# Performance work log

Hardware: AMD Instinct MI355X
Metric: run time of the kernel (lower is better)

## Reference

```python
import jax, jax.numpy as jnp
import numpy as np

EPS = 1e-3  # Keras BatchNormalization default epsilon


def _bn(x, gamma, beta, mean, var):
    # inference-mode batchnorm over channel axis 1 of [N,C,T,V]
    s = (gamma * jax.lax.rsqrt(var + EPS)).reshape(1, -1, 1, 1)
    b = (beta - gamma * mean * jax.lax.rsqrt(var + EPS)).reshape(1, -1, 1, 1)
    return x * s + b


def setup_inputs() -> dict:
    key = jax.random.key(0)
    ks = jax.random.split(key, 10)
    N, C, T, V, K, F, KT = 64, 64, 300, 25, 3, 64, 9
    x = jax.random.normal(ks[0], (N, C, T, V), jnp.float32)
    W1 = jax.random.normal(ks[1], (C, F * K), jnp.float32) * 0.05
    b1 = jnp.zeros((F * K,), jnp.float32)
    A = jax.random.normal(ks[2], (K, T, V, V), jnp.float32) * 0.2
    gamma1 = jnp.ones((F,), jnp.float32)
    beta1 = jnp.zeros((F,), jnp.float32)
    mean1 = jax.random.normal(ks[3], (F,), jnp.float32) * 0.1
    var1 = jax.random.uniform(ks[4], (F,), jnp.float32) + 0.5
    Wt = jax.random.normal(ks[5], (KT, 1, F, F), jnp.float32) * 0.05  # HWIO
    bt = jnp.zeros((F,), jnp.float32)
    gamma2 = jnp.ones((F,), jnp.float32)
    beta2 = jnp.zeros((F,), jnp.float32)
    mean2 = jax.random.normal(ks[6], (F,), jnp.float32) * 0.1
    var2 = jax.random.uniform(ks[7], (F,), jnp.float32) + 0.5
    return dict(x=x, W1=W1, b1=b1, A=A, gamma1=gamma1, beta1=beta1,
                mean1=mean1, var1=var1, Wt=Wt, bt=bt, gamma2=gamma2,
                beta2=beta2, mean2=mean2, var2=var2)


def reference(x, W1, b1, A, gamma1, beta1, mean1, var1, Wt, bt,
              gamma2, beta2, mean2, var2):
    N, C, T, V = x.shape
    K = A.shape[0]
    F = W1.shape[1] // K
    # SGTACN: 1x1 conv (channels_first) == channel matmul
    y = jnp.einsum('nctv,cf->nftv', x, W1) + b1.reshape(1, -1, 1, 1)
    y = y.reshape(N, K, F, T, V)
    # spatial graph contraction with learned per-timestep adjacency
    y = jnp.einsum('nkftv,ktvw->nftw', y, A)
    # tgcn: BN -> relu -> temporal conv [9,1] SAME -> BN
    y = jax.nn.relu(_bn(y, gamma1, beta1, mean1, var1))
    y = jax.lax.conv_general_dilated(
        y, Wt, window_strides=(1, 1), padding='SAME',
        dimension_numbers=('NCHW', 'HWIO', 'NCHW')) + bt.reshape(1, -1, 1, 1)
    y = _bn(y, gamma2, beta2, mean2, var2)
    # identity residual (stride=1, no downsample, C_in == filters) + relu
    return jax.nn.relu(y + x)
```

## Files before the change

### kernel.cpp

```cpp
#include <hip/hip_runtime.h>
#include <hip/hip_bf16.h>
#include <stdint.h>

#define EPS 1e-3f

typedef __attribute__((ext_vector_type(8))) short bf16x8;
typedef __attribute__((ext_vector_type(4))) float f32x4;

__device__ inline uint32_t pk2(float a, float b) {
    __hip_bfloat162 p;
    p.x = __float2bfloat16(a);
    p.y = __float2bfloat16(b);
    return *(uint32_t*)&p;
}

__global__ __launch_bounds__(256) void k0_prep_small(
    const float* __restrict__ W1, const float* __restrict__ Wt,
    const float* __restrict__ A,
    uint16_t* __restrict__ W1t, uint16_t* __restrict__ Abf,
    float* __restrict__ csA_g)
{
    int i = blockIdx.x * 256 + threadIdx.x;
    if (i < 12288) {
        int f = i / 192, Kp = i % 192, k = Kp >> 6, c = Kp & 63;
        __hip_bfloat16 b = __float2bfloat16(W1[c * 192 + k * 64 + f]);
        W1t[i] = *(uint16_t*)&b;
    } else if (i < 49152) {
        int j = i - 12288;
        int jj = j & 7, fo = (j >> 3) & 63, kb = j >> 9;
        int kk = kb * 8 + jj, dt = kk >> 6, fi = kk & 63;
        __hip_bfloat16 b = __float2bfloat16(Wt[(dt * 64 + fi) * 64 + fo]);
        Abf[j] = *(uint16_t*)&b;
    } else if (i < 71652) {
        int j = i - 49152;
        int k = j / 7500, r = j % 7500;
        int t = r / 25, w = r % 25;
        float s = 0.f;
        for (int v = 0; v < 25; ++v)
            s += A[((k * 300 + t) * 25 + v) * 25 + w];
        csA_g[j] = s;
    }
}

__global__ __launch_bounds__(256) void k0_prep_At(
    const float* __restrict__ A, uint16_t* __restrict__ At_g)
{
    int i = blockIdx.x * 256 + threadIdx.x;
    if (i < 921600) {
        int v = i & 31, w = (i >> 5) & 31, rest = i >> 10;
        int t = rest % 300, k = rest / 300;
        float val = 0.f;
        if (v < 25 && w < 25)
            val = A[((k * 300 + t) * 25 + v) * 25 + w];
        __hip_bfloat16 b = __float2bfloat16(val);
        At_g[i] = *(uint16_t*)&b;
    }
}

#define K1_SMEM 39680
__global__ __launch_bounds__(256, 4) void k1_fused(
    const float* __restrict__ x, const uint16_t* __restrict__ At_g,
    const uint16_t* __restrict__ W1t, const float* __restrict__ csA_g,
    const float* __restrict__ b1,
    const float* __restrict__ gamma1, const float* __restrict__ beta1,
    const float* __restrict__ mean1, const float* __restrict__ var1,
    uint32_t* __restrict__ h2u)
{
    extern __shared__ __align__(16) char smem[];
    float* s1s   = (float*)(smem + 38400);
    float* b1ns  = (float*)(smem + 38656);
    float* b1s   = (float*)(smem + 38912);

    const int t0   = blockIdx.x * 4;
    const int n    = blockIdx.y;
    const int tid  = threadIdx.x;
    const int lane = tid & 63, wv = tid >> 6;
    const int l15  = lane & 15, g = lane >> 4;
    const int t    = t0 + wv;

    bf16x8 bfr[6];
    #pragma unroll
    for (int nf = 0; nf < 6; ++nf) {
        const int col = nf * 16 + l15;
        const int k = col >> 5, w = col & 31;
        bfr[nf] = *(const bf16x8*)(At_g + (((k * 300 + t) * 32 + w) * 32 + g * 8));
    }

    const float* xb = x + (size_t)n * 480000 + t * 25;
    bf16x8 a[4];
    #pragma unroll
    for (int mf = 0; mf < 4; ++mf) {
        const int c = l15 + 16 * mf;
        const float* xr = xb + (size_t)c * 7500;
        union { bf16x8 v; uint32_t u[4]; } ua;
        if (g < 3) {
            const float* p = xr + g * 8;
            ua.u[0] = pk2(p[0], p[1]);
            ua.u[1] = pk2(p[2], p[3]);
            ua.u[2] = pk2(p[4], p[5]);
            ua.u[3] = pk2(p[6], p[7]);
        } else {
            ua.u[0] = pk2(xr[24], 0.f);
            ua.u[1] = 0; ua.u[2] = 0; ua.u[3] = 0;
        }
        a[mf] = ua.v;
    }

    if (tid < 64) {
        float rs = rsqrtf(var1[tid] + EPS);
        s1s[tid]  = gamma1[tid] * rs;
        b1ns[tid] = beta1[tid] - gamma1[tid] * mean1[tid] * rs;
    }
    if (tid >= 64 && tid < 256) b1s[tid - 64] = b1[tid - 64];

    f32x4 acc[4][6];
    #pragma unroll
    for (int mf = 0; mf < 4; ++mf)
        #pragma unroll
        for (int nf = 0; nf < 6; ++nf)
            acc[mf][nf] = (f32x4){0.f, 0.f, 0.f, 0.f};

    #pragma unroll
    for (int nf = 0; nf < 6; ++nf) {
        acc[0][nf] = __builtin_amdgcn_mfma_f32_16x16x32_bf16(a[0], bfr[nf], acc[0][nf], 0, 0, 0);
        acc[1][nf] = __builtin_amdgcn_mfma_f32_16x16x32_bf16(a[1], bfr[nf], acc[1][nf], 0, 0, 0);
        acc[2][nf] = __builtin_amdgcn_mfma_f32_16x16x32_bf16(a[2], bfr[nf], acc[2][nf], 0, 0, 0);
        acc[3][nf] = __builtin_amdgcn_mfma_f32_16x16x32_bf16(a[3], bfr[nf], acc[3][nf], 0, 0, 0);
    }

    #pragma unroll
    for (int nf = 0; nf < 6; ++nf) {
        const int col = nf * 16 + l15;
        const int k = col >> 5, w = col & 31;
        if (w < 25) {
            const int colrow = wv * 25 + w;
            const int sw = (w & 7) << 4;
            #pragma unroll
            for (int mf = 0; mf < 4; ++mf) {
                const int c0 = mf * 16 + g * 4;
                const int off = colrow * 384 + (((k * 64 + c0) * 2) ^ sw);
                uint2 val;
                val.x = pk2(acc[mf][nf][0], acc[mf][nf][1]);
                val.y = pk2(acc[mf][nf][2], acc[mf][nf][3]);
                *(uint2*)(smem + off) = val;
            }
        }
    }
    __syncthreads();

    int colv[2], coladdr[2], swz[2];
    const int nq = (wv < 3) ? 2 : 1;
    #pragma unroll
    for (int q = 0; q < 2; ++q) {
        int fr  = wv + 4 * q;
        int col = fr * 16 + l15;
        colv[q] = col;
        int colc = (col < 100) ? col : 99;
        coladdr[q] = colc * 384;
        swz[q] = ((colc % 25) & 7) << 4;
    }

    f32x4 accz[4][2];
    #pragma unroll
    for (int mf = 0; mf < 4; ++mf)
        #pragma unroll
        for (int q = 0; q < 2; ++q)
            accz[mf][q] = (f32x4){0.f, 0.f, 0.f, 0.f};

    #pragma unroll
    for (int kb = 0; kb < 6; ++kb) {
        bf16x8 az[4];
        #pragma unroll
        for (int mf = 0; mf < 4; ++mf)
            az[mf] = *(const bf16x8*)(W1t + (l15 + 16 * mf) * 192 + kb * 32 + g * 8);
        #pragma unroll
        for (int q = 0; q < 2; ++q) {
            if (q < nq) {
                bf16x8 b = *(const bf16x8*)(smem + coladdr[q] + ((kb * 64 + g * 16) ^ swz[q]));
                accz[0][q] = __builtin_amdgcn_mfma_f32_16x16x32_bf16(az[0], b, accz[0][q], 0, 0, 0);
                accz[1][q] = __builtin_amdgcn_mfma_f32_16x16x32_bf16(az[1], b, accz[1][q], 0, 0, 0);
                accz[2][q] = __builtin_amdgcn_mfma_f32_16x16x32_bf16(az[2], b, accz[2][q], 0, 0, 0);
                accz[3][q] = __builtin_amdgcn_mfma_f32_16x16x32_bf16(az[3], b, accz[3][q], 0, 0, 0);
            }
        }
    }

    const uint32_t hbase = (uint32_t)(n * 300 + t0) * 800;
    const int csbase = t0 * 25;
    #pragma unroll
    for (int q = 0; q < 2; ++q) {
        if (q < nq) {
            const int col = colv[q];
            if (col < 100) {
                const int trel = col / 25, w = col - trel * 25;
                const float cs0 = csA_g[csbase + col];
                const float cs1 = csA_g[7500 + csbase + col];
                const float cs2 = csA_g[15000 + csbase + col];
                const uint32_t rowbase = hbase + trel * 800 + w * 32;
                #pragma unroll
                for (int mf = 0; mf < 4; ++mf) {
                    const int f0 = mf * 16 + g * 4;
                    float zz[4];
                    #pragma unroll
                    for (int rg = 0; rg < 4; ++rg) {
                        const int f = f0 + rg;
                        float z = accz[mf][q][rg]
                                + b1s[f] * cs0 + b1s[64 + f] * cs1 + b1s[128 + f] * cs2;
                        z = z * s1s[f] + b1ns[f];
                        zz[rg] = fmaxf(z, 0.f);
                    }
                    uint2 st;
                    st.x = pk2(zz[0], zz[1]);
                    st.y = pk2(zz[2], zz[3]);
                    *(uint2*)(h2u + rowbase + (f0 >> 1)) = st;
                }
            }
        }
    }
}

#define K2_SMEM 51712
__global__ __launch_bounds__(256, 3) void k2_mfma(
    const char* __restrict__ h2b,
    const uint16_t* __restrict__ Abf,
    const float* __restrict__ bt,
    const float* __restrict__ gamma2, const float* __restrict__ beta2,
    const float* __restrict__ mean2,  const float* __restrict__ var2,
    const float* __restrict__ x,
    float* __restrict__ out)
{
    extern __shared__ __align__(16) char smem2[];
    char*  lds_h = smem2;
    float* s2s   = (float*)(smem2 + 51200);
    float* b2s   = s2s + 64;

    const int t0  = blockIdx.x * 8;
    const int n   = blockIdx.y;
    const int tid = threadIdx.x;

    if (tid < 64) {
        float rs = rsqrtf(var2[tid] + EPS);
        float s  = gamma2[tid] * rs;
        s2s[tid] = s;
        b2s[tid] = beta2[tid] - gamma2[tid] * mean2[tid] * rs + bt[tid] * s;
    }

    const size_t hn = (size_t)n * 300 * 3200;
    for (int c = tid; c < 3200; c += 256) {
        int rr = c >> 3, c8 = c & 7;
        int trow = rr / 25;
        int w = rr - trow * 25;
        int tg = t0 - 4 + trow;
        int4 v = make_int4(0, 0, 0, 0);
        if (tg >= 0 && tg < 300)
            v = *(const int4*)(h2b + hn + (size_t)tg * 3200 + w * 128 + (c8 << 4));
        int s = c << 4;
        *(int4*)(lds_h + (s ^ (((s >> 7) & 7) << 4))) = v;
    }
    __syncthreads();

    const int wv = tid >> 6, lane = tid & 63;
    const int l15 = lane & 15, g = lane >> 4;
    const int nMf = (wv == 0) ? 4 : 3;

    int rbase[4];
    #pragma unroll
    for (int q = 0; q < 4; ++q) {
        int col = (q * 4 + wv) * 16 + l15;
        rbase[q] = (col < 200) ? col : 199;
    }

    f32x4 acc[4][4];
    #pragma unroll
    for (int q = 0; q < 4; ++q)
        #pragma unroll
        for (int mf = 0; mf < 4; ++mf)
            acc[q][mf] = (f32x4){0.f, 0.f, 0.f, 0.f};

    for (int kk = 0; kk < 18; ++kk) {
        const int dt   = kk >> 1;
        const int half = (kk & 1) << 6;
        const int kb   = kk * 4 + g;
        bf16x8 wfr[4];
        #pragma unroll
        for (int mf = 0; mf < 4; ++mf)
            wfr[mf] = *(const bf16x8*)(Abf + (kb * 64 + l15 + mf * 16) * 8);
        #pragma unroll
        for (int q = 0; q < 4; ++q) {
            if (q < nMf) {
                int r = rbase[q] + 25 * dt;
                int s = (r << 7) + half + (g << 4);
                bf16x8 hfr = *(const bf16x8*)(lds_h + (s ^ ((r & 7) << 4)));
                acc[q][0] = __builtin_amdgcn_mfma_f32_16x16x32_bf16(hfr, wfr[0], acc[q][0], 0, 0, 0);
                acc[q][1] = __builtin_amdgcn_mfma_f32_16x16x32_bf16(hfr, wfr[1], acc[q][1], 0, 0, 0);
                acc[q][2] = __builtin_amdgcn_mfma_f32_16x16x32_bf16(hfr, wfr[2], acc[q][2], 0, 0, 0);
                acc[q][3] = __builtin_amdgcn_mfma_f32_16x16x32_bf16(hfr, wfr[3], acc[q][3], 0, 0, 0);
            }
        }
    }

    const size_t outn = (size_t)n * 480000;
    const int base = t0 * 25;
    const int vcols = (7500 - base < 200) ? (7500 - base) : 200;
    #pragma unroll
    for (int q = 0; q < 4; ++q) {
        if (q < nMf) {
            const int col0 = (q * 4 + wv) * 16 + g * 4;
            if (col0 < vcols) {
                #pragma unroll
                for (int mf = 0; mf < 4; ++mf) {
                    const int fo = mf * 16 + l15;
                    const size_t ga = outn + (size_t)fo * 7500 + base + col0;
                    const float4 xr = *(const float4*)(x + ga);
                    const float s2 = s2s[fo], b2 = b2s[fo];
                    float4 o;
                    o.x = fmaxf(acc[q][mf][0] * s2 + b2 + xr.x, 0.f);
                    o.y = fmaxf(acc[q][mf][1] * s2 + b2 + xr.y, 0.f);
                    o.z = fmaxf(acc[q][mf][2] * s2 + b2 + xr.z, 0.f);
                    o.w = fmaxf(acc[q][mf][3] * s2 + b2 + xr.w, 0.f);
                    *(float4*)(out + ga) = o;
                }
            }
        }
    }
}

extern "C" void kernel_launch(void* const* d_in, const int* in_sizes, int n_in,
                              void* d_out, int out_size, void* d_ws, size_t ws_size,
                              hipStream_t stream) {
    const float* x      = (const float*)d_in[0];
    const float* W1     = (const float*)d_in[1];
    const float* b1     = (const float*)d_in[2];
    const float* A      = (const float*)d_in[3];
    const float* gamma1 = (const float*)d_in[4];
    const float* beta1  = (const float*)d_in[5];
    const float* mean1  = (const float*)d_in[6];
    const float* var1   = (const float*)d_in[7];
    const float* Wt     = (const float*)d_in[8];
    const float* bt     = (const float*)d_in[9];
    const float* gamma2 = (const float*)d_in[10];
    const float* beta2  = (const float*)d_in[11];
    const float* mean2  = (const float*)d_in[12];
    const float* var2   = (const float*)d_in[13];
    float* out = (float*)d_out;

    char* ws = (char*)d_ws;
    uint32_t* h2u   = (uint32_t*)ws;
    char*     h2b   = ws;
    uint16_t* At_g  = (uint16_t*)(ws + 61440000);
    uint16_t* W1t   = (uint16_t*)(ws + 63283200);
    uint16_t* Abf   = (uint16_t*)(ws + 63307776);
    float*    csA_g = (float*)   (ws + 63381504);

    hipFuncSetAttribute((const void*)k1_fused,
                        hipFuncAttributeMaxDynamicSharedMemorySize, K1_SMEM);
    hipFuncSetAttribute((const void*)k2_mfma,
                        hipFuncAttributeMaxDynamicSharedMemorySize, K2_SMEM);

    k0_prep_small<<<280, 256, 0, stream>>>(W1, Wt, A, W1t, Abf, csA_g);
    k0_prep_At<<<3600, 256, 0, stream>>>(A, At_g);
    k1_fused<<<dim3(75, 64), 256, K1_SMEM, stream>>>(
        x, At_g, W1t, csA_g, b1, gamma1, beta1, mean1, var1, h2u);
    k2_mfma<<<dim3(38, 64), 256, K2_SMEM, stream>>>(
        h2b, Abf, bt, gamma2, beta2, mean2, var2, x, out);
}
```

Measured before the change: 422.3 us.

## Pre-convert x to bf16 MFMA-fragment layout in a separate prep kernel

Adds a k0_prep_x kernel that stages x through LDS, converts it to bf16 and writes it in the exact per-lane fragment order k1 consumes, plus a side array for the 25th joint. k1 then loads 16-byte vectors instead of doing strided scalar fp32 loads and conversions. This costs an extra pass that reads x and writes about 60 MB of workspace. The new path only runs when the workspace is large enough, otherwise the old path is kept.

```diff
diff --git a/kernel.cpp b/kernel.cpp
--- a/kernel.cpp
+++ b/kernel.cpp
@@ -57,9 +57,44 @@
     }
 }
 
+__global__ __launch_bounds__(256) void k0_prep_x(
+    const float* __restrict__ x, uint32_t* __restrict__ xfu,
+    uint16_t* __restrict__ x24)
+{
+    __shared__ uint16_t lds[64 * 252];
+    const int t0  = blockIdx.x * 10;
+    const int n   = blockIdx.y;
+    const int tid = threadIdx.x;
+    const float* xb = x + (size_t)n * 480000 + t0 * 25;
+
+    for (int i = tid; i < 8000; i += 256) {
+        int c = i / 125, r2 = i - c * 125;
+        float2 f2 = *(const float2*)(xb + (size_t)c * 7500 + r2 * 2);
+        *(uint32_t*)&lds[c * 252 + r2 * 2] = pk2(f2.x, f2.y);
+    }
+    __syncthreads();
+
+    const uint32_t obase = (uint32_t)(n * 300 + t0) * 768;
+    for (int o = tid; o < 7680; o += 256) {
+        int trel = o / 768, r = o - trel * 768;
+        int jp = r & 3, l15 = (r >> 2) & 15, q = r >> 6;
+        int gg = q % 3, mf = q / 3;
+        int c  = l15 + 16 * mf;
+        int rr = trel * 25 + gg * 8 + jp * 2;
+        uint32_t val = (uint32_t)lds[c * 252 + rr]
+                     | ((uint32_t)lds[c * 252 + rr + 1] << 16);
+        xfu[obase + trel * 768 + r] = val;
+    }
+    for (int i = tid; i < 640; i += 256) {
+        int trel = i >> 6, c = i & 63;
+        x24[(uint32_t)(n * 300 + t0 + trel) * 64 + c] = lds[c * 252 + trel * 25 + 24];
+    }
+}
+
 #define K1_SMEM 39680
-__global__ __launch_bounds__(256, 4) void k1_fused(
-    const float* __restrict__ x, const uint16_t* __restrict__ At_g,
+__global__ __launch_bounds__(256, 4) void k1_fused_xf(
+    const char* __restrict__ xfb, const uint16_t* __restrict__ x24,
+    const uint16_t* __restrict__ At_g,
     const uint16_t* __restrict__ W1t, const float* __restrict__ csA_g,
     const float* __restrict__ b1,
     const float* __restrict__ gamma1, const float* __restrict__ beta1,
@@ -86,21 +121,15 @@
         bfr[nf] = *(const bf16x8*)(At_g + (((k * 300 + t) * 32 + w) * 32 + g * 8));
     }
 
-    const float* xb = x + (size_t)n * 480000 + t * 25;
+    const uint32_t xoff = (uint32_t)(n * 300 + t) * 3072;
     bf16x8 a[4];
     #pragma unroll
     for (int mf = 0; mf < 4; ++mf) {
-        const int c = l15 + 16 * mf;
-        const float* xr = xb + (size_t)c * 7500;
         union { bf16x8 v; uint32_t u[4]; } ua;
         if (g < 3) {
-            const float* p = xr + g * 8;
-            ua.u[0] = pk2(p[0], p[1]);
-            ua.u[1] = pk2(p[2], p[3]);
-            ua.u[2] = pk2(p[4], p[5]);
-            ua.u[3] = pk2(p[6], p[7]);
+            ua.v = *(const bf16x8*)(xfb + xoff + (((mf * 3 + g) * 16 + l15) << 4));
         } else {
-            ua.u[0] = pk2(xr[24], 0.f);
+            ua.u[0] = (uint32_t)x24[(uint32_t)(n * 300 + t) * 64 + l15 + 16 * mf];
             ua.u[1] = 0; ua.u[2] = 0; ua.u[3] = 0;
         }
         a[mf] = ua.v;
@@ -219,6 +248,167 @@
     }
 }
 
+__global__ __launch_bounds__(256, 4) void k1_fused(
+    const float* __restrict__ x, const uint16_t* __restrict__ At_g,
+    const uint16_t* __restrict__ W1t, const float* __restrict__ csA_g,
+    const float* __restrict__ b1,
+    const float* __restrict__ gamma1, const float* __restrict__ beta1,
+    const float* __restrict__ mean1, const float* __restrict__ var1,
+    uint32_t* __restrict__ h2u)
+{
+    extern __shared__ __align__(16) char smem[];
+    float* s1s   = (float*)(smem + 38400);
+    float* b1ns  = (float*)(smem + 38656);
+    float* b1s   = (float*)(smem + 38912);
+
+    const int t0   = blockIdx.x * 4;
+    const int n    = blockIdx.y;
+    const int tid  = threadIdx.x;
+    const int lane = tid & 63, wv = tid >> 6;
+    const int l15  = lane & 15, g = lane >> 4;
+    const int t    = t0 + wv;
+
+    bf16x8 bfr[6];
+    #pragma unroll
+    for (int nf = 0; nf < 6; ++nf) {
+        const int col = nf * 16 + l15;
+        const int k = col >> 5, w = col & 31;
+        bfr[nf] = *(const bf16x8*)(At_g + (((k * 300 + t) * 32 + w) * 32 + g * 8));
+    }
+
+    const float* xb = x + (size_t)n * 480000 + t * 25;
+    bf16x8 a[4];
+    #pragma unroll
+    for (int mf = 0; mf < 4; ++mf) {
+        const int c = l15 + 16 * mf;
+        const float* xr = xb + (size_t)c * 7500;
+        union { bf16x8 v; uint32_t u[4]; } ua;
+        if (g < 3) {
+            const float* p = xr + g * 8;
+            ua.u[0] = pk2(p[0], p[1]);
+            ua.u[1] = pk2(p[2], p[3]);
+            ua.u[2] = pk2(p[4], p[5]);
+            ua.u[3] = pk2(p[6], p[7]);
+        } else {
+            ua.u[0] = pk2(xr[24], 0.f);
+            ua.u[1] = 0; ua.u[2] = 0; ua.u[3] = 0;
+        }
+        a[mf] = ua.v;
+    }
+
+    if (tid < 64) {
+        float rs = rsqrtf(var1[tid] + EPS);
+        s1s[tid]  = gamma1[tid] * rs;
+        b1ns[tid] = beta1[tid] - gamma1[tid] * mean1[tid] * rs;
+    }
+    if (tid >= 64 && tid < 256) b1s[tid - 64] = b1[tid - 64];
+
+    f32x4 acc[4][6];
+    #pragma unroll
+    for (int mf = 0; mf < 4; ++mf)
+        #pragma unroll
+        for (int nf = 0; nf < 6; ++nf)
+            acc[mf][nf] = (f32x4){0.f, 0.f, 0.f, 0.f};
+
+    #pragma unroll
+    for (int nf = 0; nf < 6; ++nf) {
+        acc[0][nf] = __builtin_amdgcn_mfma_f32_16x16x32_bf16(a[0], bfr[nf], acc[0][nf], 0, 0, 0);
+        acc[1][nf] = __builtin_amdgcn_mfma_f32_16x16x32_bf16(a[1], bfr[nf], acc[1][nf], 0, 0, 0);
+        acc[2][nf] = __builtin_amdgcn_mfma_f32_16x16x32_bf16(a[2], bfr[nf], acc[2][nf], 0, 0, 0);
+        acc[3][nf] = __builtin_amdgcn_mfma_f32_16x16x32_bf16(a[3], bfr[nf], acc[3][nf], 0, 0, 0);
+    }
+
+    #pragma unroll
+    for (int nf = 0; nf < 6; ++nf) {
+        const int col = nf * 16 + l15;
+        const int k = col >> 5, w = col & 31;
+        if (w < 25) {
+            const int colrow = wv * 25 + w;
+            const int sw = (w & 7) << 4;
+            #pragma unroll
+            for (int mf = 0; mf < 4; ++mf) {
+                const int c0 = mf * 16 + g * 4;
+                const int off = colrow * 384 + (((k * 64 + c0) * 2) ^ sw);
+                uint2 val;
+                val.x = pk2(acc[mf][nf][0], acc[mf][nf][1]);
+                val.y = pk2(acc[mf][nf][2], acc[mf][nf][3]);
+                *(uint2*)(smem + off) = val;
+            }
+        }
+    }
+    __syncthreads();
+
+    int colv[2], coladdr[2], swz[2];
+    const int nq = (wv < 3) ? 2 : 1;
+    #pragma unroll
+    for (int q = 0; q < 2; ++q) {
+        int fr  = wv + 4 * q;
+        int col = fr * 16 + l15;
+        colv[q] = col;
+        int colc = (col < 100) ? col : 99;
+        coladdr[q] = colc * 384;
+        swz[q] = ((colc % 25) & 7) << 4;
+    }
+
+    f32x4 accz[4][2];
+    #pragma unroll
+    for (int mf = 0; mf < 4; ++mf)
+        #pragma unroll
+        for (int q = 0; q < 2; ++q)
+            accz[mf][q] = (f32x4){0.f, 0.f, 0.f, 0.f};
+
+    #pragma unroll
+    for (int kb = 0; kb < 6; ++kb) {
+        bf16x8 az[4];
+        #pragma unroll
+        for (int mf = 0; mf < 4; ++mf)
+            az[mf] = *(const bf16x8*)(W1t + (l15 + 16 * mf) * 192 + kb * 32 + g * 8);
+        #pragma unroll
+        for (int q = 0; q < 2; ++q) {
+            if (q < nq) {
+                bf16x8 b = *(const bf16x8*)(smem + coladdr[q] + ((kb * 64 + g * 16) ^ swz[q]));
+                accz[0][q] = __builtin_amdgcn_mfma_f32_16x16x32_bf16(az[0], b, accz[0][q], 0, 0, 0);
+                accz[1][q] = __builtin_amdgcn_mfma_f32_16x16x32_bf16(az[1], b, accz[1][q], 0, 0, 0);
+                accz[2][q] = __builtin_amdgcn_mfma_f32_16x16x32_bf16(az[2], b, accz[2][q], 0, 0, 0);
+                accz[3][q] = __builtin_amdgcn_mfma_f32_16x16x32_bf16(az[3], b, accz[3][q], 0, 0, 0);
+            }
+        }
+    }
+
+    const uint32_t hbase = (uint32_t)(n * 300 + t0) * 800;
+    const int csbase = t0 * 25;
+    #pragma unroll
+    for (int q = 0; q < 2; ++q) {
+        if (q < nq) {
+            const int col = colv[q];
+            if (col < 100) {
+                const int trel = col / 25, w = col - trel * 25;
+                const float cs0 = csA_g[csbase + col];
+                const float cs1 = csA_g[7500 + csbase + col];
+                const float cs2 = csA_g[15000 + csbase + col];
+                const uint32_t rowbase = hbase + trel * 800 + w * 32;
+                #pragma unroll
+                for (int mf = 0; mf < 4; ++mf) {
+                    const int f0 = mf * 16 + g * 4;
+                    float zz[4];
+                    #pragma unroll
+                    for (int rg = 0; rg < 4; ++rg) {
+                        const int f = f0 + rg;
+                        float z = accz[mf][q][rg]
+                                + b1s[f] * cs0 + b1s[64 + f] * cs1 + b1s[128 + f] * cs2;
+                        z = z * s1s[f] + b1ns[f];
+                        zz[rg] = fmaxf(z, 0.f);
+                    }
+                    uint2 st;
+                    st.x = pk2(zz[0], zz[1]);
+                    st.y = pk2(zz[2], zz[3]);
+                    *(uint2*)(h2u + rowbase + (f0 >> 1)) = st;
+                }
+            }
+        }
+    }
+}
+
 #define K2_SMEM 51712
 __global__ __launch_bounds__(256, 3) void k2_mfma(
     const char* __restrict__ h2b,
@@ -343,24 +533,47 @@
     const float* mean2  = (const float*)d_in[12];
     const float* var2   = (const float*)d_in[13];
     float* out = (float*)d_out;
-
     char* ws = (char*)d_ws;
-    uint32_t* h2u   = (uint32_t*)ws;
-    char*     h2b   = ws;
-    uint16_t* At_g  = (uint16_t*)(ws + 61440000);
-    uint16_t* W1t   = (uint16_t*)(ws + 63283200);
-    uint16_t* Abf   = (uint16_t*)(ws + 63307776);
-    float*    csA_g = (float*)   (ws + 63381504);
-
+
+    hipFuncSetAttribute((const void*)k1_fused_xf,
+                        hipFuncAttributeMaxDynamicSharedMemorySize, K1_SMEM);
     hipFuncSetAttribute((const void*)k1_fused,
                         hipFuncAttributeMaxDynamicSharedMemorySize, K1_SMEM);
     hipFuncSetAttribute((const void*)k2_mfma,
                         hipFuncAttributeMaxDynamicSharedMemorySize, K2_SMEM);
 
-    k0_prep_small<<<280, 256, 0, stream>>>(W1, Wt, A, W1t, Abf, csA_g);
-    k0_prep_At<<<3600, 256, 0, stream>>>(A, At_g);
-    k1_fused<<<dim3(75, 64), 256, K1_SMEM, stream>>>(
-        x, At_g, W1t, csA_g, b1, gamma1, beta1, mean1, var1, h2u);
-    k2_mfma<<<dim3(38, 64), 256, K2_SMEM, stream>>>(
-        h2b, Abf, bt, gamma2, beta2, mean2, var2, x, out);
-}
+    const size_t NEED_XF = 124911504;
+    if (ws_size >= NEED_XF) {
+        uint32_t* h2u   = (uint32_t*)ws;
+        char*     h2b   = ws;
+        char*     xfb   = ws + 61440000;
+        uint32_t* xfu   = (uint32_t*)xfb;
+        uint16_t* x24   = (uint16_t*)(ws + 120422400);
+        uint16_t* At_g  = (uint16_t*)(ws + 122880000);
+        uint16_t* W1t   = (uint16_t*)(ws + 124723200);
+        uint16_t* Abf   = (uint16_t*)(ws + 124747776);
+        float*    csA_g = (float*)   (ws + 124821504);
+
+        k0_prep_small<<<280, 256, 0, stream>>>(W1, Wt, A, W1t, Abf, csA_g);
+        k0_prep_At<<<3600, 256, 0, stream>>>(A, At_g);
+        k0_prep_x<<<dim3(30, 64), 256, 0, stream>>>(x, xfu, x24);
+        k1_fused_xf<<<dim3(75, 64), 256, K1_SMEM, stream>>>(
+            xfb, x24, At_g, W1t, csA_g, b1, gamma1, beta1, mean1, var1, h2u);
+        k2_mfma<<<dim3(38, 64), 256, K2_SMEM, stream>>>(
+            h2b, Abf, bt, gamma2, beta2, mean2, var2, x, out);
+    } else {
+        uint32_t* h2u   = (uint32_t*)ws;
+        char*     h2b   = ws;
+        uint16_t* At_g  = (uint16_t*)(ws + 61440000);
+        uint16_t* W1t   = (uint16_t*)(ws + 63283200);
+        uint16_t* Abf   = (uint16_t*)(ws + 63307776);
+        float*    csA_g = (float*)   (ws + 63381504);
+
+        k0_prep_small<<<280, 256, 0, stream>>>(W1, Wt, A, W1t, Abf, csA_g);
+        k0_prep_At<<<3600, 256, 0, stream>>>(A, At_g);
+        k1_fused<<<dim3(75, 64), 256, K1_SMEM, stream>>>(
+            x, At_g, W1t, csA_g, b1, gamma1, beta1, mean1, var1, h2u);
+        k2_mfma<<<dim3(38, 64), 256, K2_SMEM, stream>>>(
+            h2b, Abf, bt, gamma2, beta2, mean2, var2, x, out);
+    }
+}
```

Result: slower. 461.4 us (+9.3%).

## Make k1 stage-2 wave-local with per-wave LDS slabs, splitting stage-1 accumulators

Applied to the files above, without the earlier changes.

Each wave now writes its own timestep's graph-contracted tile into a private LDS slab and then runs the W1 channel GEMM on that slab itself. The block-wide barrier between the two stages becomes a per-wave lgkmcnt wait. Stage 1 is also split into two halves of three fragments, which cuts live accumulator registers. This removes cross-wave synchronisation and the uneven 2/2/2/1 fragment split, at the cost of some padded columns (w 25..31) doing wasted MFMAs.

```diff
diff --git a/kernel.cpp b/kernel.cpp
--- a/kernel.cpp
+++ b/kernel.cpp
@@ -58,7 +58,7 @@
 }
 
 #define K1_SMEM 39680
-__global__ __launch_bounds__(256, 4) void k1_fused(
+__global__ __launch_bounds__(256, 4) void k1_wave(
     const float* __restrict__ x, const uint16_t* __restrict__ At_g,
     const uint16_t* __restrict__ W1t, const float* __restrict__ csA_g,
     const float* __restrict__ b1,
@@ -77,6 +77,7 @@
     const int lane = tid & 63, wv = tid >> 6;
     const int l15  = lane & 15, g = lane >> 4;
     const int t    = t0 + wv;
+    char* slab = smem + wv * 9600;
 
     bf16x8 bfr[6];
     #pragma unroll
@@ -112,108 +113,107 @@
         b1ns[tid] = beta1[tid] - gamma1[tid] * mean1[tid] * rs;
     }
     if (tid >= 64 && tid < 256) b1s[tid - 64] = b1[tid - 64];
-
-    f32x4 acc[4][6];
+    __syncthreads();
+
+    #pragma unroll
+    for (int hh = 0; hh < 2; ++hh) {
+        f32x4 acc[4][3];
+        #pragma unroll
+        for (int mf = 0; mf < 4; ++mf)
+            #pragma unroll
+            for (int nf3 = 0; nf3 < 3; ++nf3)
+                acc[mf][nf3] = (f32x4){0.f, 0.f, 0.f, 0.f};
+
+        #pragma unroll
+        for (int nf3 = 0; nf3 < 3; ++nf3) {
+            const int nf = hh * 3 + nf3;
+            acc[0][nf3] = __builtin_amdgcn_mfma_f32_16x16x32_bf16(a[0], bfr[nf], acc[0][nf3], 0, 0, 0);
+            acc[1][nf3] = __builtin_amdgcn_mfma_f32_16x16x32_bf16(a[1], bfr[nf], acc[1][nf3], 0, 0, 0);
+            acc[2][nf3] = __builtin_amdgcn_mfma_f32_16x16x32_bf16(a[2], bfr[nf], acc[2][nf3], 0, 0, 0);
+            acc[3][nf3] = __builtin_amdgcn_mfma_f32_16x16x32_bf16(a[3], bfr[nf], acc[3][nf3], 0, 0, 0);
+        }
+
+        #pragma unroll
+        for (int nf3 = 0; nf3 < 3; ++nf3) {
+            const int col = (hh * 3 + nf3) * 16 + l15;
+            const int k = col >> 5, w = col & 31;
+            if (w < 25) {
+                const int sw = (w & 7) << 4;
+                #pragma unroll
+                for (int mf = 0; mf < 4; ++mf) {
+                    const int c0 = mf * 16 + g * 4;
+                    const int off = w * 384 + (((k * 64 + c0) * 2) ^ sw);
+                    uint2 val;
+                    val.x = pk2(acc[mf][nf3][0], acc[mf][nf3][1]);
+                    val.y = pk2(acc[mf][nf3][2], acc[mf][nf3][3]);
+                    *(uint2*)(slab + off) = val;
+                }
+            }
+        }
+    }
+
+    asm volatile("s_waitcnt lgkmcnt(0)" ::: "memory");
+    __builtin_amdgcn_sched_barrier(0);
+
+    int wq[2], qaddr[2], qswz[2];
+    #pragma unroll
+    for (int q = 0; q < 2; ++q) {
+        int w = q * 16 + l15;
+        wq[q] = w;
+        int wc = (w < 25) ? w : 24;
+        qaddr[q] = wc * 384;
+        qswz[q]  = (wc & 7) << 4;
+    }
+
+    f32x4 accz[4][2];
     #pragma unroll
     for (int mf = 0; mf < 4; ++mf)
         #pragma unroll
-        for (int nf = 0; nf < 6; ++nf)
-            acc[mf][nf] = (f32x4){0.f, 0.f, 0.f, 0.f};
-
-    #pragma unroll
-    for (int nf = 0; nf < 6; ++nf) {
-        acc[0][nf] = __builtin_amdgcn_mfma_f32_16x16x32_bf16(a[0], bfr[nf], acc[0][nf], 0, 0, 0);
-        acc[1][nf] = __builtin_amdgcn_mfma_f32_16x16x32_bf16(a[1], bfr[nf], acc[1][nf], 0, 0, 0);
-        acc[2][nf] = __builtin_amdgcn_mfma_f32_16x16x32_bf16(a[2], bfr[nf], acc[2][nf], 0, 0, 0);
-        acc[3][nf] = __builtin_amdgcn_mfma_f32_16x16x32_bf16(a[3], bfr[nf], acc[3][nf], 0, 0, 0);
-    }
-
-    #pragma unroll
-    for (int nf = 0; nf < 6; ++nf) {
-        const int col = nf * 16 + l15;
-        const int k = col >> 5, w = col & 31;
+        for (int q = 0; q < 2; ++q)
+            accz[mf][q] = (f32x4){0.f, 0.f, 0.f, 0.f};
+
+    #pragma unroll
+    for (int kb = 0; kb < 6; ++kb) {
+        bf16x8 az[4];
+        #pragma unroll
+        for (int mf = 0; mf < 4; ++mf)
+            az[mf] = *(const bf16x8*)(W1t + (l15 + 16 * mf) * 192 + kb * 32 + g * 8);
+        #pragma unroll
+        for (int q = 0; q < 2; ++q) {
+            bf16x8 b = *(const bf16x8*)(slab + qaddr[q] + ((kb * 64 + g * 16) ^ qswz[q]));
+            accz[0][q] = __builtin_amdgcn_mfma_f32_16x16x32_bf16(az[0], b, accz[0][q], 0, 0, 0);
+            accz[1][q] = __builtin_amdgcn_mfma_f32_16x16x32_bf16(az[1], b, accz[1][q], 0, 0, 0);
+            accz[2][q] = __builtin_amdgcn_mfma_f32_16x16x32_bf16(az[2], b, accz[2][q], 0, 0, 0);
+            accz[3][q] = __builtin_amdgcn_mfma_f32_16x16x32_bf16(az[3], b, accz[3][q], 0, 0, 0);
+        }
+    }
+
+    const uint32_t tb = (uint32_t)(n * 300 + t);
+    #pragma unroll
+    for (int q = 0; q < 2; ++q) {
+        const int w = wq[q];
         if (w < 25) {
-            const int colrow = wv * 25 + w;
-            const int sw = (w & 7) << 4;
+            const int ci = t * 25 + w;
+            const float cs0 = csA_g[ci];
+            const float cs1 = csA_g[7500 + ci];
+            const float cs2 = csA_g[15000 + ci];
+            const uint32_t rowbase = tb * 800 + w * 32;
             #pragma unroll
             for (int mf = 0; mf < 4; ++mf) {
-                const int c0 = mf * 16 + g * 4;
-                const int off = colrow * 384 + (((k * 64 + c0) * 2) ^ sw);
-                uint2 val;
-                val.x = pk2(acc[mf][nf][0], acc[mf][nf][1]);
-                val.y = pk2(acc[mf][nf][2], acc[mf][nf][3]);
-                *(uint2*)(smem + off) = val;
-            }
-        }
-    }
-    __syncthreads();
-
-    int colv[2], coladdr[2], swz[2];
-    const int nq = (wv < 3) ? 2 : 1;
-    #pragma unroll
-    for (int q = 0; q < 2; ++q) {
-        int fr  = wv + 4 * q;
-        int col = fr * 16 + l15;
-        colv[q] = col;
-        int colc = (col < 100) ? col : 99;
-        coladdr[q] = colc * 384;
-        swz[q] = ((colc % 25) & 7) << 4;
-    }
-
-    f32x4 accz[4][2];
-    #pragma unroll
-    for (int mf = 0; mf < 4; ++mf)
-        #pragma unroll
-        for (int q = 0; q < 2; ++q)
-            accz[mf][q] = (f32x4){0.f, 0.f, 0.f, 0.f};
-
-    #pragma unroll
-    for (int kb = 0; kb < 6; ++kb) {
-        bf16x8 az[4];
-        #pragma unroll
-        for (int mf = 0; mf < 4; ++mf)
-            az[mf] = *(const bf16x8*)(W1t + (l15 + 16 * mf) * 192 + kb * 32 + g * 8);
-        #pragma unroll
-        for (int q = 0; q < 2; ++q) {
-            if (q < nq) {
-                bf16x8 b = *(const bf16x8*)(smem + coladdr[q] + ((kb * 64 + g * 16) ^ swz[q]));
-                accz[0][q] = __builtin_amdgcn_mfma_f32_16x16x32_bf16(az[0], b, accz[0][q], 0, 0, 0);
-                accz[1][q] = __builtin_amdgcn_mfma_f32_16x16x32_bf16(az[1], b, accz[1][q], 0, 0, 0);
-                accz[2][q] = __builtin_amdgcn_mfma_f32_16x16x32_bf16(az[2], b, accz[2][q], 0, 0, 0);
-                accz[3][q] = __builtin_amdgcn_mfma_f32_16x16x32_bf16(az[3], b, accz[3][q], 0, 0, 0);
-            }
-        }
-    }
-
-    const uint32_t hbase = (uint32_t)(n * 300 + t0) * 800;
-    const int csbase = t0 * 25;
-    #pragma unroll
-    for (int q = 0; q < 2; ++q) {
-        if (q < nq) {
-            const int col = colv[q];
-            if (col < 100) {
-                const int trel = col / 25, w = col - trel * 25;
-                const float cs0 = csA_g[csbase + col];
-                const float cs1 = csA_g[7500 + csbase + col];
-                const float cs2 = csA_g[15000 + csbase + col];
-                const uint32_t rowbase = hbase + trel * 800 + w * 32;
+                const int f0 = mf * 16 + g * 4;
+                float zz[4];
                 #pragma unroll
-                for (int mf = 0; mf < 4; ++mf) {
-                    const int f0 = mf * 16 + g * 4;
-                    float zz[4];
-                    #pragma unroll
-                    for (int rg = 0; rg < 4; ++rg) {
-                        const int f = f0 + rg;
-                        float z = accz[mf][q][rg]
-                                + b1s[f] * cs0 + b1s[64 + f] * cs1 + b1s[128 + f] * cs2;
-                        z = z * s1s[f] + b1ns[f];
-                        zz[rg] = fmaxf(z, 0.f);
-                    }
-                    uint2 st;
-                    st.x = pk2(zz[0], zz[1]);
-                    st.y = pk2(zz[2], zz[3]);
-                    *(uint2*)(h2u + rowbase + (f0 >> 1)) = st;
+                for (int rg = 0; rg < 4; ++rg) {
+                    const int f = f0 + rg;
+                    float z = accz[mf][q][rg]
+                            + b1s[f] * cs0 + b1s[64 + f] * cs1 + b1s[128 + f] * cs2;
+                    z = z * s1s[f] + b1ns[f];
+                    zz[rg] = fmaxf(z, 0.f);
                 }
+                uint2 st;
+                st.x = pk2(zz[0], zz[1]);
+                st.y = pk2(zz[2], zz[3]);
+                *(uint2*)(h2u + rowbase + (f0 >> 1)) = st;
             }
         }
     }
@@ -352,14 +352,14 @@
     uint16_t* Abf   = (uint16_t*)(ws + 63307776);
     float*    csA_g = (float*)   (ws + 63381504);
 
-    hipFuncSetAttribute((const void*)k1_fused,
+    hipFuncSetAttribute((const void*)k1_wave,
                         hipFuncAttributeMaxDynamicSharedMemorySize, K1_SMEM);
     hipFuncSetAttribute((const void*)k2_mfma,
                         hipFuncAttributeMaxDynamicSharedMemorySize, K2_SMEM);
 
     k0_prep_small<<<280, 256, 0, stream>>>(W1, Wt, A, W1t, Abf, csA_g);
     k0_prep_At<<<3600, 256, 0, stream>>>(A, At_g);
-    k1_fused<<<dim3(75, 64), 256, K1_SMEM, stream>>>(
+    k1_wave<<<dim3(75, 64), 256, K1_SMEM, stream>>>(
         x, At_g, W1t, csA_g, b1, gamma1, beta1, mean1, var1, h2u);
     k2_mfma<<<dim3(38, 64), 256, K2_SMEM, stream>>>(
         h2b, Abf, bt, gamma2, beta2, mean2, var2, x, out);
```

Measured after the change: 418.2 us. About the same (-1.0%).
